# Performance work log

Hardware: AMD Instinct MI355X
Metric: run time of the kernel (lower is better)

## Reference

```python
import jax, jax.numpy as jnp
import numpy as np
from jax import lax

B, T, K = 2048, 1024, 8  # batch, max seq len, num_tags


def setup_inputs() -> dict:
    key = jax.random.key(0)
    k1, k2, k3, k4, k5, k6, k7 = jax.random.split(key, 7)
    score = jax.random.normal(k1, (B, T, K), jnp.float32)
    log_p = jax.nn.log_softmax(jax.random.normal(k2, (B, T, K), jnp.float32), axis=-1)
    tags = jax.random.randint(k3, (B, T), 0, K)
    seq_l = jax.random.randint(k4, (B,), 1, T + 1)  # valid lengths in [1, T]
    transitions = jax.random.normal(k5, (K, K), jnp.float32) * 0.1
    start_transitions = jax.random.normal(k6, (K,), jnp.float32) * 0.1
    end_transitions = jax.random.normal(k7, (K,), jnp.float32) * 0.1
    return {
        "log_p": log_p,
        "score": score,
        "transitions": transitions,
        "start_transitions": start_transitions,
        "end_transitions": end_transitions,
        "tags": tags,
        "seq_l": seq_l,
    }


def _crf_nll(score, tags, mask, transitions, start_transitions, end_transitions):
    """Linear-chain CRF negative log-likelihood, summed over the batch.
    score: [B,T,K] emissions; tags: [B,T] gold; mask: [B,T] bool."""
    maskf = mask.astype(score.dtype)

    # ---- numerator: score of the gold tag path ----
    emit = jnp.take_along_axis(score, tags[..., None], axis=-1)[..., 0]  # [B,T]
    num = (emit * maskf).sum(-1)
    num = num + start_transitions[tags[:, 0]]
    trans_sc = transitions[tags[:, :-1], tags[:, 1:]]  # [B,T-1]
    num = num + (trans_sc * maskf[:, 1:]).sum(-1)
    last_idx = (mask.sum(-1).astype(jnp.int32) - 1)  # [B]
    last_tag = jnp.take_along_axis(tags, last_idx[:, None], axis=1)[:, 0]
    num = num + end_transitions[last_tag]

    # ---- denominator: log partition via log-sum-exp scan over time ----
    alpha0 = start_transitions[None, :] + score[:, 0]  # [B,K]

    def step(alpha, xs):
        emit_t, mask_t = xs  # [B,K], [B]
        # alpha[b,i] + transitions[i,j] + emit[b,j], logsumexp over i
        nxt = jax.nn.logsumexp(alpha[:, :, None] + transitions[None, :, :], axis=1) + emit_t
        alpha = jnp.where(mask_t[:, None], nxt, alpha)  # freeze past end-of-seq
        return alpha, None

    xs = (jnp.swapaxes(score[:, 1:], 0, 1), jnp.swapaxes(mask[:, 1:], 0, 1))
    alpha, _ = lax.scan(step, alpha0, xs)
    log_z = jax.nn.logsumexp(alpha + end_transitions[None, :], axis=-1)  # [B]

    return -(num - log_z).sum()


def reference(log_p, score, transitions, start_transitions, end_transitions, tags, seq_l):
    mask = jnp.arange(T)[None, :] < seq_l[:, None]  # [B,T] bool
    loss = _crf_nll(score, tags, mask, transitions, start_transitions, end_transitions) / B
    # training path: quick predictions = argmax over per-token log_p, zero-padded
    pred_idx = jnp.argmax(log_p, axis=-1) * mask.astype(jnp.int64)
    return loss, pred_idx
```

## Files before the change

kernel.cpp:

```cpp
#include <hip/hip_runtime.h>
#include <hip/hip_bf16.h>


namespace {

constexpr int B = 2048;
constexpr int T = 1024;

__device__ __forceinline__ float max8(const float* a) {
  return fmaxf(fmaxf(fmaxf(a[0], a[1]), fmaxf(a[2], a[3])),
               fmaxf(fmaxf(a[4], a[5]), fmaxf(a[6], a[7])));
}

__global__ __launch_bounds__(256) void pred_num_kernel(
    const float* __restrict__ log_p, const float* __restrict__ score,
    const float* __restrict__ trans, const float* __restrict__ start_tr,
    const float* __restrict__ end_tr, const int* __restrict__ tags,
    const int* __restrict__ seq_l, float* __restrict__ out_pred,
    float* __restrict__ ws_num) {
  int g = blockIdx.x * blockDim.x + threadIdx.x;
  int b = g >> 10;
  int t = g & (T - 1);

  const float4* lp = reinterpret_cast<const float4*>(log_p) + (g << 1);
  float4 u0 = lp[0], u1 = lp[1];
  float v[8] = {u0.x, u0.y, u0.z, u0.w, u1.x, u1.y, u1.z, u1.w};
  int best = 0;
  float bv = v[0];
#pragma unroll
  for (int j = 1; j < 8; ++j) {
    if (v[j] > bv) { bv = v[j]; best = j; }
  }

  int L = seq_l[b];
  bool act = (t < L);
  out_pred[g] = act ? (float)best : 0.0f;

  float contrib = 0.0f;
  if (act) {
    int tg = tags[g];
    contrib = score[g * 8 + tg];
    if (t == 0)
      contrib += start_tr[tg];
    else
      contrib += trans[tags[g - 1] * 8 + tg];
    if (t == L - 1) contrib += end_tr[tg];
  }
#pragma unroll
  for (int off = 32; off >= 1; off >>= 1) contrib += __shfl_down(contrib, off);
  if ((threadIdx.x & 63) == 0) atomicAdd(&ws_num[b], contrib);
}

template <int NC>
__global__ __launch_bounds__(256) void chunk_kernel(
    const float* __restrict__ score, const float* __restrict__ trans,
    const int* __restrict__ seq_l, float* __restrict__ wsA,
    float* __restrict__ wsS) {
  constexpr int CL = T / NC;
  int g = blockIdx.x * blockDim.x + threadIdx.x;
  int k = g & 7;
  int c = (g >> 3) & (NC - 1);
  int b = g >> 3 >>  (NC == 32 ? 5 : 4);

  float E[8][8];
#pragma unroll
  for (int i = 0; i < 8; ++i)
#pragma unroll
    for (int j = 0; j < 8; ++j) E[i][j] = __expf(trans[i * 8 + j]);

  float a[8];
#pragma unroll
  for (int j = 0; j < 8; ++j) a[j] = (j == k) ? 1.0f : 0.0f;
  float sig = 0.0f;

  int L = seq_l[b];
  int t0 = c * CL;
  int ts = (c == 0) ? 1 : t0;
  int te = min(t0 + CL, L);
  int n = te - ts;
  const float* sp = score + ((size_t)b * T + ts) * 8;

  for (int it = 0; it < n; ++it) {
    float4 sA = *reinterpret_cast<const float4*>(sp);
    float4 sB = *reinterpret_cast<const float4*>(sp + 4);
    sp += 8;
    float em[8] = {__expf(sA.x), __expf(sA.y), __expf(sA.z), __expf(sA.w),
                   __expf(sB.x), __expf(sB.y), __expf(sB.z), __expf(sB.w)};
    float na[8];
#pragma unroll
    for (int j = 0; j < 8; ++j) {
      float acc = E[0][j] * a[0];
#pragma unroll
      for (int i = 1; i < 8; ++i) acc = fmaf(E[i][j], a[i], acc);
      na[j] = em[j] * acc;
    }
#pragma unroll
    for (int j = 0; j < 8; ++j) a[j] = na[j];
    if ((it & 7) == 7) {
      float mm = max8(a);
      float r = __builtin_amdgcn_rcpf(mm);
#pragma unroll
      for (int j = 0; j < 8; ++j) a[j] *= r;
      sig += __logf(mm);
    }
  }
  {
    float mm = max8(a);
    if (mm > 0.0f) {
      float r = __builtin_amdgcn_rcpf(mm);
#pragma unroll
      for (int j = 0; j < 8; ++j) a[j] *= r;
      sig += __logf(mm);
    }
  }

  float* Ao = wsA + (size_t)(b * NC + c) * 64;
#pragma unroll
  for (int j = 0; j < 8; ++j) Ao[j * 8 + k] = a[j];
  wsS[(b * NC + c) * 8 + k] = sig;
}

template <int NC>
__global__ __launch_bounds__(256) void combine_kernel(
    const float* __restrict__ score, const float* __restrict__ start_tr,
    const float* __restrict__ end_tr, const float* __restrict__ wsA,
    const float* __restrict__ wsS, const float* __restrict__ ws_num,
    float* __restrict__ out_loss) {
  int tid = blockIdx.x * blockDim.x + threadIdx.x;
  int j = tid & 7;
  int b = tid >> 3;

  float pj = __expf(start_tr[j] + score[(size_t)b * T * 8 + j]);
  float mm = pj;
#pragma unroll
  for (int m = 1; m < 8; m <<= 1) mm = fmaxf(mm, __shfl_xor(mm, m, 8));
  float tau = __logf(mm);
  pj *= __builtin_amdgcn_rcpf(mm);

  float eej = __expf(end_tr[j]);

  for (int c = 0; c < NC; ++c) {
    const float* Ab = wsA + (size_t)(b * NC + c) * 64;
    float sgj = wsS[(b * NC + c) * 8 + j];
    float smax = sgj;
#pragma unroll
    for (int m = 1; m < 8; m <<= 1) smax = fmaxf(smax, __shfl_xor(smax, m, 8));
    float wj = pj * __expf(sgj - smax);
    float w[8];
#pragma unroll
    for (int i = 0; i < 8; ++i) w[i] = __shfl(wj, i, 8);
    float4 r0 = *reinterpret_cast<const float4*>(Ab + j * 8);
    float4 r1 = *reinterpret_cast<const float4*>(Ab + j * 8 + 4);
    float acc = r0.x * w[0];
    acc = fmaf(r0.y, w[1], acc);
    acc = fmaf(r0.z, w[2], acc);
    acc = fmaf(r0.w, w[3], acc);
    acc = fmaf(r1.x, w[4], acc);
    acc = fmaf(r1.y, w[5], acc);
    acc = fmaf(r1.z, w[6], acc);
    acc = fmaf(r1.w, w[7], acc);
    float mm2 = acc;
#pragma unroll
    for (int m = 1; m < 8; m <<= 1) mm2 = fmaxf(mm2, __shfl_xor(mm2, m, 8));
    tau += smax + __logf(mm2);
    pj = acc * __builtin_amdgcn_rcpf(mm2);
  }

  float term = pj * eej;
#pragma unroll
  for (int m = 1; m < 8; m <<= 1) term += __shfl_xor(term, m, 8);
  float logz = tau + __logf(term);

  float part = (j == 0) ? (logz - ws_num[b]) * (1.0f / (float)B) : 0.0f;
#pragma unroll
  for (int off = 32; off >= 1; off >>= 1) part += __shfl_down(part, off);
  if ((threadIdx.x & 63) == 0) atomicAdd(out_loss, part);
}

}

extern "C" void kernel_launch(void* const* d_in, const int* in_sizes, int n_in,
                              void* d_out, int out_size, void* d_ws,
                              size_t ws_size, hipStream_t stream) {
  const float* log_p = (const float*)d_in[0];
  const float* score = (const float*)d_in[1];
  const float* trans = (const float*)d_in[2];
  const float* start_tr = (const float*)d_in[3];
  const float* end_tr = (const float*)d_in[4];
  const int* tags = (const int*)d_in[5];
  const int* seq_l = (const int*)d_in[6];
  float* out = (float*)d_out;

  size_t need32 = ((size_t)B * 32 * 72 + B) * sizeof(float);
  bool use32 = ws_size >= need32;
  int nc = use32 ? 32 : 16;

  float* wsA = (float*)d_ws;
  float* wsS = wsA + (size_t)B * nc * 64;
  float* wsNum = wsS + (size_t)B * nc * 8;

  hipMemsetAsync(wsNum, 0, B * sizeof(float), stream);
  hipMemsetAsync(out, 0, sizeof(float), stream);

  pred_num_kernel<<<(B * T) / 256, 256, 0, stream>>>(
      log_p, score, trans, start_tr, end_tr, tags, seq_l, out + 1, wsNum);
  if (use32) {
    chunk_kernel<32><<<(B * 32 * 8) / 256, 256, 0, stream>>>(score, trans,
                                                             seq_l, wsA, wsS);
    combine_kernel<32><<<(B * 8) / 256, 256, 0, stream>>>(
        score, start_tr, end_tr, wsA, wsS, wsNum, out);
  } else {
    chunk_kernel<16><<<(B * 16 * 8) / 256, 256, 0, stream>>>(score, trans,
                                                             seq_l, wsA, wsS);
    combine_kernel<16><<<(B * 8) / 256, 256, 0, stream>>>(
        score, start_tr, end_tr, wsA, wsS, wsNum, out);
  }
}
```

Baseline: 220.8 us.

## Raise chunk count to 64, prefetch loads, and process four tokens per thread

Doubles the number of time chunks in the chunked CRF forward pass when workspace permits, shortening each thread's serial recurrence in exchange for a longer combine loop and more workspace traffic. Adds software prefetching of the next emission row in the chunk kernel and of the next chunk matrix in the combine kernel to hide load latency. The pred/numerator kernel now handles four tokens per thread with vectorized loads, cutting thread count and per-token reduction overhead. If the workspace is too small, it falls back to 32 chunks instead of 16.

```diff
diff --git a/kernel.cpp b/kernel.cpp
--- a/kernel.cpp
+++ b/kernel.cpp
@@ -18,40 +18,52 @@
     const float* __restrict__ end_tr, const int* __restrict__ tags,
     const int* __restrict__ seq_l, float* __restrict__ out_pred,
     float* __restrict__ ws_num) {
-  int g = blockIdx.x * blockDim.x + threadIdx.x;
-  int b = g >> 10;
-  int t = g & (T - 1);
-
-  const float4* lp = reinterpret_cast<const float4*>(log_p) + (g << 1);
-  float4 u0 = lp[0], u1 = lp[1];
-  float v[8] = {u0.x, u0.y, u0.z, u0.w, u1.x, u1.y, u1.z, u1.w};
-  int best = 0;
-  float bv = v[0];
-#pragma unroll
-  for (int j = 1; j < 8; ++j) {
-    if (v[j] > bv) { bv = v[j]; best = j; }
-  }
-
+  int tid = blockIdx.x * blockDim.x + threadIdx.x;
+  int g0 = tid << 2;
+  int b = g0 >> 10;
+  int t0 = g0 & (T - 1);
   int L = seq_l[b];
-  bool act = (t < L);
-  out_pred[g] = act ? (float)best : 0.0f;
+
+  const float4* lp = reinterpret_cast<const float4*>(log_p) + (g0 << 1);
+  float4 u[8];
+#pragma unroll
+  for (int r = 0; r < 8; ++r) u[r] = lp[r];
+  int4 tg4 = *reinterpret_cast<const int4*>(tags + g0);
+  int tg[4] = {tg4.x, tg4.y, tg4.z, tg4.w};
+  int prev0 = (t0 == 0) ? 0 : tags[g0 - 1];
 
   float contrib = 0.0f;
-  if (act) {
-    int tg = tags[g];
-    contrib = score[g * 8 + tg];
-    if (t == 0)
-      contrib += start_tr[tg];
-    else
-      contrib += trans[tags[g - 1] * 8 + tg];
-    if (t == L - 1) contrib += end_tr[tg];
+#pragma unroll
+  for (int r = 0; r < 4; ++r) {
+    float v[8] = {u[2 * r].x, u[2 * r].y, u[2 * r].z, u[2 * r].w,
+                  u[2 * r + 1].x, u[2 * r + 1].y, u[2 * r + 1].z,
+                  u[2 * r + 1].w};
+    int best = 0;
+    float bv = v[0];
+#pragma unroll
+    for (int j = 1; j < 8; ++j) {
+      if (v[j] > bv) { bv = v[j]; best = j; }
+    }
+    int t = t0 + r;
+    bool act = (t < L);
+    out_pred[g0 + r] = act ? (float)best : 0.0f;
+    if (act) {
+      int tgr = tg[r];
+      float csum = score[(size_t)(g0 + r) * 8 + tgr];
+      if (t == 0)
+        csum += start_tr[tgr];
+      else
+        csum += trans[((r == 0) ? prev0 : tg[r - 1]) * 8 + tgr];
+      if (t == L - 1) csum += end_tr[tgr];
+      contrib += csum;
+    }
   }
 #pragma unroll
   for (int off = 32; off >= 1; off >>= 1) contrib += __shfl_down(contrib, off);
   if ((threadIdx.x & 63) == 0) atomicAdd(&ws_num[b], contrib);
 }
 
-template <int NC>
+template <int NC, int LOG_NC>
 __global__ __launch_bounds__(256) void chunk_kernel(
     const float* __restrict__ score, const float* __restrict__ trans,
     const int* __restrict__ seq_l, float* __restrict__ wsA,
@@ -60,7 +72,7 @@
   int g = blockIdx.x * blockDim.x + threadIdx.x;
   int k = g & 7;
   int c = (g >> 3) & (NC - 1);
-  int b = g >> 3 >>  (NC == 32 ? 5 : 4);
+  int b = g >> (3 + LOG_NC);
 
   float E[8][8];
 #pragma unroll
@@ -80,9 +92,17 @@
   int n = te - ts;
   const float* sp = score + ((size_t)b * T + ts) * 8;
 
+  float4 nA, nB;
+  if (n > 0) {
+    nA = *reinterpret_cast<const float4*>(sp);
+    nB = *reinterpret_cast<const float4*>(sp + 4);
+  }
   for (int it = 0; it < n; ++it) {
-    float4 sA = *reinterpret_cast<const float4*>(sp);
-    float4 sB = *reinterpret_cast<const float4*>(sp + 4);
+    float4 sA = nA, sB = nB;
+    if (it + 1 < n) {
+      nA = *reinterpret_cast<const float4*>(sp + 8);
+      nB = *reinterpret_cast<const float4*>(sp + 12);
+    }
     sp += 8;
     float em[8] = {__expf(sA.x), __expf(sA.y), __expf(sA.z), __expf(sA.w),
                    __expf(sB.x), __expf(sB.y), __expf(sB.z), __expf(sB.w)};
@@ -139,26 +159,36 @@
 
   float eej = __expf(end_tr[j]);
 
+  const float* Ab = wsA + (size_t)b * NC * 64;
+  const float* Sb = wsS + (size_t)b * NC * 8;
+  float4 r0 = *reinterpret_cast<const float4*>(Ab + j * 8);
+  float4 r1 = *reinterpret_cast<const float4*>(Ab + j * 8 + 4);
+  float sgj = Sb[j];
+
   for (int c = 0; c < NC; ++c) {
-    const float* Ab = wsA + (size_t)(b * NC + c) * 64;
-    float sgj = wsS[(b * NC + c) * 8 + j];
-    float smax = sgj;
+    float4 c0 = r0, c1 = r1;
+    float sj = sgj;
+    if (c + 1 < NC) {
+      const float* An = Ab + (size_t)(c + 1) * 64;
+      r0 = *reinterpret_cast<const float4*>(An + j * 8);
+      r1 = *reinterpret_cast<const float4*>(An + j * 8 + 4);
+      sgj = Sb[(c + 1) * 8 + j];
+    }
+    float smax = sj;
 #pragma unroll
     for (int m = 1; m < 8; m <<= 1) smax = fmaxf(smax, __shfl_xor(smax, m, 8));
-    float wj = pj * __expf(sgj - smax);
+    float wj = pj * __expf(sj - smax);
     float w[8];
 #pragma unroll
     for (int i = 0; i < 8; ++i) w[i] = __shfl(wj, i, 8);
-    float4 r0 = *reinterpret_cast<const float4*>(Ab + j * 8);
-    float4 r1 = *reinterpret_cast<const float4*>(Ab + j * 8 + 4);
-    float acc = r0.x * w[0];
-    acc = fmaf(r0.y, w[1], acc);
-    acc = fmaf(r0.z, w[2], acc);
-    acc = fmaf(r0.w, w[3], acc);
-    acc = fmaf(r1.x, w[4], acc);
-    acc = fmaf(r1.y, w[5], acc);
-    acc = fmaf(r1.z, w[6], acc);
-    acc = fmaf(r1.w, w[7], acc);
+    float acc = c0.x * w[0];
+    acc = fmaf(c0.y, w[1], acc);
+    acc = fmaf(c0.z, w[2], acc);
+    acc = fmaf(c0.w, w[3], acc);
+    acc = fmaf(c1.x, w[4], acc);
+    acc = fmaf(c1.y, w[5], acc);
+    acc = fmaf(c1.z, w[6], acc);
+    acc = fmaf(c1.w, w[7], acc);
     float mm2 = acc;
 #pragma unroll
     for (int m = 1; m < 8; m <<= 1) mm2 = fmaxf(mm2, __shfl_xor(mm2, m, 8));
@@ -191,10 +221,10 @@
   const int* seq_l = (const int*)d_in[6];
   float* out = (float*)d_out;
 
-  size_t need32 = ((size_t)B * 32 * 72 + B) * sizeof(float);
-  bool use32 = ws_size >= need32;
-  int nc = use32 ? 32 : 16;
-
+  size_t need64 = ((size_t)B * 64 * 72 + B) * sizeof(float);
+  bool use64 = ws_size >= need64;
+
+  int nc = use64 ? 64 : 32;
   float* wsA = (float*)d_ws;
   float* wsS = wsA + (size_t)B * nc * 64;
   float* wsNum = wsS + (size_t)B * nc * 8;
@@ -202,17 +232,17 @@
   hipMemsetAsync(wsNum, 0, B * sizeof(float), stream);
   hipMemsetAsync(out, 0, sizeof(float), stream);
 
-  pred_num_kernel<<<(B * T) / 256, 256, 0, stream>>>(
+  pred_num_kernel<<<(B * T / 4) / 256, 256, 0, stream>>>(
       log_p, score, trans, start_tr, end_tr, tags, seq_l, out + 1, wsNum);
-  if (use32) {
-    chunk_kernel<32><<<(B * 32 * 8) / 256, 256, 0, stream>>>(score, trans,
-                                                             seq_l, wsA, wsS);
+  if (use64) {
+    chunk_kernel<64, 6><<<(B * 64 * 8) / 256, 256, 0, stream>>>(
+        score, trans, seq_l, wsA, wsS);
+    combine_kernel<64><<<(B * 8) / 256, 256, 0, stream>>>(
+        score, start_tr, end_tr, wsA, wsS, wsNum, out);
+  } else {
+    chunk_kernel<32, 5><<<(B * 32 * 8) / 256, 256, 0, stream>>>(
+        score, trans, seq_l, wsA, wsS);
     combine_kernel<32><<<(B * 8) / 256, 256, 0, stream>>>(
         score, start_tr, end_tr, wsA, wsS, wsNum, out);
-  } else {
-    chunk_kernel<16><<<(B * 16 * 8) / 256, 256, 0, stream>>>(score, trans,
-                                                             seq_l, wsA, wsS);
-    combine_kernel<16><<<(B * 8) / 256, 256, 0, stream>>>(
-        score, start_tr, end_tr, wsA, wsS, wsNum, out);
-  }
-}
+  }
+}
```

After: 236.7 us. 7.2% more time.
